# Performance work log

Hardware: AMD Instinct MI355X
Metric: run time of the kernel (lower is better)

The kernel has to match this reference:

```python
import jax, jax.numpy as jnp
import numpy as np

B, S, HID = 1, 2048, 2048
H, KV, D = 16, 4, 128  # head_dim = HID // H; GQA group size g = H // KV
THETA = 10000.0


def setup_inputs() -> dict:
    key = jax.random.key(0)
    ks = jax.random.split(key, 5)
    s = 0.02  # initializer_range
    return {
        "hidden_states": jax.random.normal(ks[0], (B, S, HID), jnp.float32),
        "wq": jax.random.normal(ks[1], (HID, H * D), jnp.float32) * s,
        "wk": jax.random.normal(ks[2], (HID, KV * D), jnp.float32) * s,
        "wv": jax.random.normal(ks[3], (HID, KV * D), jnp.float32) * s,
        "wo": jax.random.normal(ks[4], (H * D, HID), jnp.float32) * s,
        "attention_mask": jnp.ones((B, S), jnp.int32),
        "position_ids": jnp.broadcast_to(jnp.arange(S, dtype=jnp.int32), (B, S)),
    }


def _rope(x, position_ids):
    # x: [b, s, h, d]; rotate consecutive (even, odd) pairs by angle t * theta^{-2j/d}
    half = D // 2
    inv_freq = 1.0 / (THETA ** (jnp.arange(0, D, 2, dtype=jnp.float32) / D))  # [half]
    ang = position_ids[..., None].astype(jnp.float32) * inv_freq  # [b, s, half]
    cos = jnp.cos(ang)[:, :, None, :]  # [b, s, 1, half]
    sin = jnp.sin(ang)[:, :, None, :]
    xr = x.astype(jnp.float32).reshape(*x.shape[:-1], half, 2)
    x0, x1 = xr[..., 0], xr[..., 1]
    out = jnp.stack((x0 * cos - x1 * sin, x0 * sin + x1 * cos), axis=-1)
    return out.reshape(x.shape)


def reference(hidden_states, wq, wk, wv, wo, attention_mask, position_ids):
    b, s, _ = hidden_states.shape
    g = H // KV
    xq = (hidden_states @ wq).reshape(b, s, H, D)
    xk = (hidden_states @ wk).reshape(b, s, KV, D)
    xv = (hidden_states @ wv).reshape(b, s, KV, D)
    # GQA: each kv head repeated g consecutive times -> H heads (matches einops '(h g)')
    xk = jnp.repeat(xk, g, axis=2)
    xv = jnp.repeat(xv, g, axis=2)
    xq = _rope(xq, position_ids)
    xk = _rope(xk, position_ids)
    # causal + padding mask -> additive bias (0 or -inf), softmax in fp32
    causal = jnp.tril(jnp.ones((s, s), dtype=bool))[None, None]  # [1,1,q,k]
    mask = causal & (attention_mask[:, None, None, :] > 0)  # [b,1,q,k]
    scores = jnp.einsum('bqhd,bkhd->bhqk', xq.astype(jnp.float32), xk.astype(jnp.float32))
    scores = scores / jnp.sqrt(jnp.float32(D))
    scores = jnp.where(mask, scores, jnp.finfo(jnp.float32).min)
    attn_weights = jax.nn.softmax(scores, axis=-1)  # [b,h,q,k] fp32
    attn = jnp.einsum('bhqk,bkhd->bqhd', attn_weights, xv.astype(jnp.float32))
    return (attn.reshape(b, s, H * D).astype(hidden_states.dtype)) @ wo
```

## Files before the change

kernel.cpp:

```cpp
#include <hip/hip_runtime.h>
#include <hip/hip_bf16.h>

#define S_LEN 2048
#define HIDDIM 2048
#define NH 16
#define NKV 4
#define HD 128
#define KVROW 1024
#define QKVN 3072

typedef __attribute__((ext_vector_type(8))) short short8;
typedef __attribute__((ext_vector_type(8))) unsigned short ushort8;
typedef __attribute__((ext_vector_type(4))) float f32x4;

__device__ __forceinline__ unsigned short f2bf(float f) {
  union { float f; unsigned int u; } v; v.f = f;
  unsigned int r = (v.u + 0x7FFFu + ((v.u >> 16) & 1u)) >> 16;
  return (unsigned short)r;
}
__device__ __forceinline__ float bf2f(unsigned short h) {
  union { unsigned int u; float f; } v; v.u = ((unsigned int)h) << 16;
  return v.f;
}

__device__ __forceinline__ void gl2lds16(const unsigned short* src,
                                         unsigned short* dst) {
  __builtin_amdgcn_global_load_lds(
      (const __attribute__((address_space(1))) unsigned int*)src,
      (__attribute__((address_space(3))) unsigned int*)dst, 16, 0, 0);
}

__device__ __forceinline__ void tw_body(
    const float* __restrict__ W, unsigned short* __restrict__ Wt,
    int Nsrc, int Kdst, int n_off, int bx, int by, int tid,
    unsigned short (*Ts)[72]) {
  const int n0 = bx * 64, k0 = by * 64;
  const int c2 = (tid & 31) * 2, rb = tid >> 5;
#pragma unroll
  for (int p = 0; p < 8; ++p) {
    int r = rb + p * 8;
    float2 v = *(const float2*)&W[(size_t)(k0 + r) * Nsrc + n0 + c2];
    Ts[c2][r] = f2bf(v.x);
    Ts[c2 + 1][r] = f2bf(v.y);
  }
  __syncthreads();
  const int n = tid >> 2, kq = (tid & 3) * 16;
  ushort8 w0 = *(const ushort8*)&Ts[n][kq];
  ushort8 w1 = *(const ushort8*)&Ts[n][kq + 8];
  size_t base = (size_t)(n_off + n0 + n) * Kdst + k0 + kq;
  *(ushort8*)&Wt[base] = w0;
  *(ushort8*)&Wt[base + 8] = w1;
}

__global__ __launch_bounds__(256) void prep_kernel(
    const float* __restrict__ H, unsigned short* __restrict__ Hb,
    const float* __restrict__ wq, const float* __restrict__ wk,
    const float* __restrict__ wv, unsigned short* __restrict__ WT1,
    const int* __restrict__ amask, unsigned* __restrict__ mb) {
  __shared__ unsigned short Ts[64][72];
  const int b = (int)blockIdx.x, tid = threadIdx.x;
  if (b < 2048) {
    int i = (b * 256 + tid) * 8;
    float4 a = *(const float4*)(H + i), c = *(const float4*)(H + i + 4);
    ushort8 r;
    r[0] = f2bf(a.x); r[1] = f2bf(a.y); r[2] = f2bf(a.z); r[3] = f2bf(a.w);
    r[4] = f2bf(c.x); r[5] = f2bf(c.y); r[6] = f2bf(c.z); r[7] = f2bf(c.w);
    *(ushort8*)(Hb + i) = r;
  } else if (b < 3072) {
    int t = b - 2048;
    tw_body(wq, WT1, HIDDIM, HIDDIM, 0, t & 31, t >> 5, tid, Ts);
  } else if (b < 3328) {
    int t = b - 3072;
    tw_body(wk, WT1, 512, HIDDIM, 2048, t & 7, t >> 3, tid, Ts);
  } else if (b < 3584) {
    int t = b - 3328;
    tw_body(wv, WT1, 512, HIDDIM, 2560, t & 7, t >> 3, tid, Ts);
  } else {
    if (tid < 64) {
      unsigned m = 0;
#pragma unroll
      for (int i = 0; i < 32; ++i) m |= (amask[tid * 32 + i] != 0 ? 1u : 0u) << i;
      mb[tid] = m;
    }
  }
}

__global__ __launch_bounds__(256) void transpose_w(
    const float* __restrict__ W, unsigned short* __restrict__ Wt,
    int Nsrc, int Kdst, int n_off) {
  __shared__ unsigned short Ts[64][72];
  tw_body(W, Wt, Nsrc, Kdst, n_off, (int)blockIdx.x, (int)blockIdx.y,
          (int)threadIdx.x, Ts);
}

__global__ __launch_bounds__(256) void tvrope_kernel(
    unsigned short* __restrict__ Qb, unsigned short* __restrict__ KVb,
    unsigned short* __restrict__ Vt, const int* __restrict__ pos) {
  __shared__ unsigned short Ts[64][72];
  const int b = (int)blockIdx.x, tid = threadIdx.x;
  if (b < 256) {
    const int c0 = (b & 7) * 64, s0 = (b >> 3) * 64;
    const int sr = tid >> 2, cq = (tid & 3) * 16;
    ushort8 a = *(const ushort8*)&KVb[(size_t)(s0 + sr) * KVROW + 512 + c0 + cq];
    ushort8 c = *(const ushort8*)&KVb[(size_t)(s0 + sr) * KVROW + 512 + c0 + cq + 8];
#pragma unroll
    for (int j = 0; j < 8; ++j) { Ts[cq + j][sr] = a[j]; Ts[cq + 8 + j][sr] = c[j]; }
    __syncthreads();
    const int cc = tid >> 2, sq = (tid & 3) * 16;
    ushort8 w0 = *(const ushort8*)&Ts[cc][sq];
    ushort8 w1 = *(const ushort8*)&Ts[cc][sq + 8];
    *(ushort8*)&Vt[(size_t)(c0 + cc) * S_LEN + s0 + sq] = w0;
    *(ushort8*)&Vt[(size_t)(c0 + cc) * S_LEN + s0 + sq + 8] = w1;
  } else {
    int idx = (b - 256) * 256 + tid;
    int s = idx >> 6, j = idx & 63;
    float inv = exp2f(-0.2076205059304703f * (float)j);
    float ang = (float)pos[s] * inv;
    float sn, cs;
    __sincosf(ang, &sn, &cs);
    auto rot = [&](unsigned short* base) {
      unsigned* p = (unsigned*)base;
      unsigned v = *p;
      float x0 = bf2f((unsigned short)(v & 0xffff));
      float x1 = bf2f((unsigned short)(v >> 16));
      unsigned r = (unsigned)f2bf(x0 * cs - x1 * sn) |
                   ((unsigned)f2bf(x0 * sn + x1 * cs) << 16);
      *p = r;
    };
#pragma unroll
    for (int hh = 0; hh < NH; ++hh) rot(Qb + (size_t)s * HIDDIM + hh * HD + 2 * j);
#pragma unroll
    for (int hh = 0; hh < NKV; ++hh) rot(KVb + (size_t)s * KVROW + hh * HD + 2 * j);
  }
}

template <bool CF>
__global__ __launch_bounds__(256) void gemm_tn(
    const unsigned short* __restrict__ A, const unsigned short* __restrict__ Bt,
    void* __restrict__ C1, void* __restrict__ C2,
    int M, int N, int K, int splitcol, int ld1, int ld2) {
  __shared__ unsigned short As[2][128 * 64];
  __shared__ unsigned short Bs[2][64 * 64];
  const int m0 = blockIdx.y * 128, n0 = blockIdx.x * 64;
  const int tid = threadIdx.x, wid = tid >> 6, lane = tid & 63;
  const int wr = wid >> 1, wc = wid & 1;
  const int lr = lane & 15, lg = lane >> 4;

  f32x4 acc[4][2];
#pragma unroll
  for (int m = 0; m < 4; ++m)
#pragma unroll
    for (int n = 0; n < 2; ++n) acc[m][n] = (f32x4){0.f, 0.f, 0.f, 0.f};

  const int srow = lane >> 3;
  const int scolb = (lane & 7) << 4;
  auto stage = [&](int k0, int b) {
#pragma unroll
    for (int j = 0; j < 4; ++j) {
      int row = wid * 32 + j * 8 + srow;
      int src = (scolb ^ ((row & 7) << 4)) >> 1;
      gl2lds16(A + (size_t)(m0 + row) * K + k0 + src,
               &As[b][(wid * 32 + j * 8) * 64]);
    }
#pragma unroll
    for (int j = 0; j < 2; ++j) {
      int row = wid * 16 + j * 8 + srow;
      int src = (scolb ^ ((row & 7) << 4)) >> 1;
      gl2lds16(Bt + (size_t)(n0 + row) * K + k0 + src,
               &Bs[b][(wid * 16 + j * 8) * 64]);
    }
  };

  stage(0, 0);
  int cur = 0;
  for (int k0 = 0; k0 < K; k0 += 64) {
    __syncthreads();
    if (k0 + 64 < K) stage(k0 + 64, cur ^ 1);
#pragma unroll
    for (int s = 0; s < 2; ++s) {
      short8 af[4], bfv[2];
#pragma unroll
      for (int m = 0; m < 4; ++m) {
        int row = wr * 64 + m * 16 + lr;
        int off = ((s * 64 + lg * 16) ^ ((row & 7) << 4)) >> 1;
        af[m] = *(const short8*)&As[cur][row * 64 + off];
      }
#pragma unroll
      for (int n = 0; n < 2; ++n) {
        int row = wc * 32 + n * 16 + lr;
        int off = ((s * 64 + lg * 16) ^ ((row & 7) << 4)) >> 1;
        bfv[n] = *(const short8*)&Bs[cur][row * 64 + off];
      }
#pragma unroll
      for (int m = 0; m < 4; ++m)
#pragma unroll
        for (int n = 0; n < 2; ++n)
          acc[m][n] = __builtin_amdgcn_mfma_f32_16x16x32_bf16(af[m], bfv[n], acc[m][n], 0, 0, 0);
    }
    cur ^= 1;
  }

#pragma unroll
  for (int m = 0; m < 4; ++m)
#pragma unroll
    for (int n = 0; n < 2; ++n)
#pragma unroll
      for (int r = 0; r < 4; ++r) {
        int row = m0 + wr * 64 + m * 16 + lg * 4 + r;
        int col = n0 + wc * 32 + n * 16 + lr;
        float v = acc[m][n][r];
        if (CF) ((float*)C1)[(size_t)row * ld1 + col] = v;
        else if (col < splitcol) ((unsigned short*)C1)[(size_t)row * ld1 + col] = f2bf(v);
        else ((unsigned short*)C2)[(size_t)row * ld2 + (col - splitcol)] = f2bf(v);
      }
}

__global__ __launch_bounds__(256) void attn_kernel(
    const unsigned short* __restrict__ Qb, const unsigned short* __restrict__ KVb,
    const unsigned short* __restrict__ VtG, const unsigned* __restrict__ mbits,
    unsigned short* __restrict__ Ob,
    unsigned short* __restrict__ Opart, float* __restrict__ Lpart, int nsplit) {
  const int x = (int)blockIdx.x;
  const int qt = 63 - (x >> 2);
  const int c = x & 3;
  const int kvh = (int)blockIdx.y;
  const int nch = (qt >> 4) + 1;
  if (nsplit == 0) { if (c != 0) return; }
  else if (c >= nch) return;
  const int qb = qt * 32;
  int kbeg = 0, kend = qb + 32;
  bool partial = false;
  if (nsplit && nch > 1) {
    kbeg = c * 512;
    kend = min(kend, kbeg + 512);
    partial = true;
  }

  __shared__ unsigned short Klds[2][32 * 128];
  __shared__ unsigned short Vlds[2][128 * 32];
  const int tid = threadIdx.x, wid = tid >> 6, lane = tid & 63;
  const int lr = lane & 15, lg = lane >> 4;
  const int h = kvh * 4 + wid;

  short8 qfa[4], qfb[4];
  {
    const unsigned short* qpa = Qb + (size_t)(qb + lr) * HIDDIM + h * HD;
    const unsigned short* qpb = Qb + (size_t)(qb + 16 + lr) * HIDDIM + h * HD;
#pragma unroll
    for (int cc = 0; cc < 4; ++cc) {
      qfa[cc] = *(const short8*)(qpa + cc * 32 + lg * 8);
      qfb[cc] = *(const short8*)(qpb + cc * 32 + lg * 8);
    }
  }
  f32x4 oa[8], ob[8];
#pragma unroll
  for (int cc = 0; cc < 8; ++cc) {
    oa[cc] = (f32x4){0.f, 0.f, 0.f, 0.f};
    ob[cc] = (f32x4){0.f, 0.f, 0.f, 0.f};
  }
  float lsa = 0.f, lsb = 0.f;

  const unsigned short* Vg = VtG + (size_t)(kvh * HD) * S_LEN;

  const int ksr_ = lane >> 4;
  const int kscb = (lane & 15) << 4;
  const int vsr_ = lane >> 2;
  const int vscb = (lane & 3) << 4;

  auto stage = [&](int kt, int b) {
#pragma unroll
    for (int j = 0; j < 2; ++j) {
      int krow = wid * 8 + j * 4 + ksr_;
      int ksrc = (kscb ^ ((krow & 7) << 4)) >> 1;
      gl2lds16(KVb + (size_t)(kt + krow) * KVROW + kvh * HD + ksrc,
               &Klds[b][(wid * 8 + j * 4) * 128]);
      int vrow = wid * 32 + j * 16 + vsr_;
      int vsrc = (vscb ^ ((vrow & 3) << 4)) >> 1;
      gl2lds16(Vg + (size_t)vrow * S_LEN + kt + vsrc,
               &Vlds[b][(wid * 32 + j * 16) * 32]);
    }
  };

  stage(kbeg, 0);

  const int qra = qb + lr, qrb = qb + 16 + lr;
  const float SCALE = 0.08838834764831845f;
  int cur = 0;

  const int s0 = lr + ((lg & 1) << 5);
  const int s1 = s0 + 16;
  const bool lo = (lg < 2);
  auto exchange = [&](const float p[2][4]) -> short8 {
    unsigned W0 = (unsigned)f2bf(p[0][0]) | ((unsigned)f2bf(p[0][1]) << 16);
    unsigned W1 = (unsigned)f2bf(p[0][2]) | ((unsigned)f2bf(p[0][3]) << 16);
    unsigned W2 = (unsigned)f2bf(p[1][0]) | ((unsigned)f2bf(p[1][1]) << 16);
    unsigned W3 = (unsigned)f2bf(p[1][2]) | ((unsigned)f2bf(p[1][3]) << 16);
    unsigned x0 = __shfl(W0, s0, 64), y0 = __shfl(W2, s0, 64);
    unsigned x1 = __shfl(W1, s0, 64), y1 = __shfl(W3, s0, 64);
    unsigned x2 = __shfl(W0, s1, 64), y2 = __shfl(W2, s1, 64);
    unsigned x3 = __shfl(W1, s1, 64), y3 = __shfl(W3, s1, 64);
    union { unsigned u[4]; short8 s8; } pu;
    pu.u[0] = lo ? x0 : y0;
    pu.u[1] = lo ? x1 : y1;
    pu.u[2] = lo ? x2 : y2;
    pu.u[3] = lo ? x3 : y3;
    return pu.s8;
  };

  for (int kt = kbeg; kt < kend; kt += 32) {
    __syncthreads();
    if (kt + 32 < kend) stage(kt + 32, cur ^ 1);

    f32x4 sa[2], sb[2];
#pragma unroll
    for (int t = 0; t < 2; ++t) {
      sa[t] = (f32x4){0.f, 0.f, 0.f, 0.f};
      sb[t] = (f32x4){0.f, 0.f, 0.f, 0.f};
    }
    const unsigned short* kbase = &Klds[cur][0];
    __builtin_amdgcn_s_setprio(1);
#pragma unroll
    for (int t = 0; t < 2; ++t)
#pragma unroll
      for (int cc = 0; cc < 4; ++cc) {
        short8 kf = *(const short8*)(kbase + ((t * 16 + lr) << 7) +
                                     ((((cc << 6) + (lg << 4)) ^ ((lr & 7) << 4)) >> 1));
        sa[t] = __builtin_amdgcn_mfma_f32_16x16x32_bf16(kf, qfa[cc], sa[t], 0, 0, 0);
        sb[t] = __builtin_amdgcn_mfma_f32_16x16x32_bf16(kf, qfb[cc], sb[t], 0, 0, 0);
      }
    __builtin_amdgcn_s_setprio(0);
    const unsigned mw = mbits[kt >> 5];
    float pa[2][4], pb[2][4];
    if ((kt + 31 <= qb) && (mw == ~0u)) {
#pragma unroll
      for (int t = 0; t < 2; ++t)
#pragma unroll
        for (int r = 0; r < 4; ++r) {
          float va = __expf(sa[t][r] * SCALE - 3.0f);
          float vb = __expf(sb[t][r] * SCALE - 3.0f);
          pa[t][r] = va; lsa += va;
          pb[t][r] = vb; lsb += vb;
        }
    } else {
#pragma unroll
      for (int t = 0; t < 2; ++t)
#pragma unroll
        for (int r = 0; r < 4; ++r) {
          int kk = t * 16 + lg * 4 + r;
          bool okm = (mw >> kk) & 1u;
          float va = __expf((okm && kt + kk <= qra) ? sa[t][r] * SCALE - 3.0f : -1e30f);
          float vb = __expf((okm && kt + kk <= qrb) ? sb[t][r] * SCALE - 3.0f : -1e30f);
          pa[t][r] = va; lsa += va;
          pb[t][r] = vb; lsb += vb;
        }
    }
    short8 pfa = exchange(pa);
    short8 pfb = exchange(pb);
    const unsigned short* vbase = &Vlds[cur][0];
    __builtin_amdgcn_s_setprio(1);
#pragma unroll
    for (int cc = 0; cc < 8; ++cc) {
      short8 vf = *(const short8*)(vbase + ((cc * 16 + lr) << 5) +
                                   ((lg ^ (lr & 3)) << 3));
      oa[cc] = __builtin_amdgcn_mfma_f32_16x16x32_bf16(pfa, vf, oa[cc], 0, 0, 0);
      ob[cc] = __builtin_amdgcn_mfma_f32_16x16x32_bf16(pfb, vf, ob[cc], 0, 0, 0);
    }
    __builtin_amdgcn_s_setprio(0);
    cur ^= 1;
  }

  float la = lsa;
  la += __shfl_xor(la, 16, 64);
  la += __shfl_xor(la, 32, 64);
  float lb = lsb;
  lb += __shfl_xor(lb, 16, 64);
  lb += __shfl_xor(lb, 32, 64);

  if (!partial) {
    float lra[4], lrb[4];
#pragma unroll
    for (int r = 0; r < 4; ++r) {
      lra[r] = 1.0f / __shfl(la, lg * 4 + r, 16);
      lrb[r] = 1.0f / __shfl(lb, lg * 4 + r, 16);
    }
#pragma unroll
    for (int cc = 0; cc < 8; ++cc)
#pragma unroll
      for (int r = 0; r < 4; ++r) {
        const int rowa = qb + lg * 4 + r;
        const int rowb = qb + 16 + lg * 4 + r;
        Ob[(size_t)rowa * HIDDIM + h * HD + cc * 16 + lr] = f2bf(oa[cc][r] * lra[r]);
        Ob[(size_t)rowb * HIDDIM + h * HD + cc * 16 + lr] = f2bf(ob[cc][r] * lrb[r]);
      }
  } else {
    const int g = qt >> 4, j = qt & 15;
    const int base = (g == 1) ? 0 : (g == 2) ? 32 : 80;
    const int slot = base + j * nch + c + 144 * kvh;
    if (lg == 0) {
      Lpart[slot * 128 + wid * 32 + lr] = la;
      Lpart[slot * 128 + wid * 32 + 16 + lr] = lb;
    }
#pragma unroll
    for (int cc = 0; cc < 8; ++cc)
#pragma unroll
      for (int r = 0; r < 4; ++r) {
        Opart[(size_t)slot * 16384 + wid * 4096 +
              (lg * 4 + r) * 128 + cc * 16 + lr] = f2bf(oa[cc][r]);
        Opart[(size_t)slot * 16384 + wid * 4096 +
              (16 + lg * 4 + r) * 128 + cc * 16 + lr] = f2bf(ob[cc][r]);
      }
  }
}

__global__ __launch_bounds__(256) void combine_kernel(
    const unsigned short* __restrict__ Opart, const float* __restrict__ Lpart,
    unsigned short* __restrict__ Ab) {
  const int qt = 16 + (int)blockIdx.x;
  const int kvh = (int)blockIdx.y;
  const int nch = (qt >> 4) + 1;
  const int g = qt >> 4, j = qt & 15;
  const int base = (g == 1) ? 0 : (g == 2) ? 32 : 80;
  const int s0 = base + j * nch + 144 * kvh;
  const int tid = threadIdx.x;
  const int rowid = tid >> 1;
  const int d0 = (tid & 1) * 64;
  float L = 0.f;
  for (int cc = 0; cc < nch; ++cc) L += Lpart[(s0 + cc) * 128 + rowid];
  const float linv = 1.0f / L;
  const int h = kvh * 4 + (rowid >> 5);
  const int row = qt * 32 + (rowid & 31);
  unsigned short* dst = Ab + (size_t)row * HIDDIM + h * HD + d0;
  for (int i = 0; i < 64; i += 8) {
    float acc[8] = {0, 0, 0, 0, 0, 0, 0, 0};
    for (int cc = 0; cc < nch; ++cc) {
      ushort8 v = *(const ushort8*)&Opart[(size_t)(s0 + cc) * 16384 +
                                          rowid * 128 + d0 + i];
#pragma unroll
      for (int k = 0; k < 8; ++k) acc[k] += bf2f(v[k]);
    }
    ushort8 r;
#pragma unroll
    for (int k = 0; k < 8; ++k) r[k] = f2bf(acc[k] * linv);
    *(ushort8*)(dst + i) = r;
  }
}

extern "C" void kernel_launch(void* const* d_in, const int* in_sizes, int n_in,
                              void* d_out, int out_size, void* d_ws, size_t ws_size,
                              hipStream_t stream) {
  const float* hidden = (const float*)d_in[0];
  const float* wq = (const float*)d_in[1];
  const float* wk = (const float*)d_in[2];
  const float* wv = (const float*)d_in[3];
  const float* wo = (const float*)d_in[4];
  const int* amask = (const int*)d_in[5];
  const int* pos = (const int*)d_in[6];

  unsigned short* Qb = (unsigned short*)d_ws;
  unsigned short* KVb = Qb + (size_t)S_LEN * HIDDIM;
  unsigned short* Ab = KVb + (size_t)S_LEN * KVROW;
  unsigned short* WT1 = Ab + (size_t)S_LEN * HIDDIM;
  unsigned short* Hb = WT1 + (size_t)QKVN * HIDDIM;
  float* out = (float*)d_out;

  unsigned short* Opart = WT1;
  unsigned short* Vt_chunk = WT1 + (size_t)576 * 16384;
  unsigned* mbits_chunk = (unsigned*)((char*)d_ws + 41943040ull);
  float* Lpart = (float*)((char*)d_ws + 41943296ull);
  const size_t need_chunk = 42238208ull;
  unsigned short* Vt_fb = WT1 + (size_t)HIDDIM * HIDDIM;
  unsigned* mbits_fb = (unsigned*)((char*)d_ws + 31457280ull);

  const int nsplit = (ws_size >= need_chunk) ? 1 : 0;
  unsigned short* Vt = nsplit ? Vt_chunk : Vt_fb;
  unsigned* mbits = nsplit ? mbits_chunk : mbits_fb;

  dim3 blk(256);
  prep_kernel<<<3585, blk, 0, stream>>>(hidden, Hb, wq, wk, wv, WT1, amask, mbits);
  gemm_tn<false><<<dim3(QKVN / 64, S_LEN / 128), blk, 0, stream>>>(
      Hb, WT1, Qb, KVb, S_LEN, QKVN, HIDDIM, 2048, HIDDIM, KVROW);
  tvrope_kernel<<<768, blk, 0, stream>>>(Qb, KVb, Vt, pos);
  attn_kernel<<<dim3(256, NKV), blk, 0, stream>>>(
      Qb, KVb, Vt, mbits, Ab, Opart, Lpart, nsplit);
  if (nsplit)
    combine_kernel<<<dim3(48, NKV), blk, 0, stream>>>(Opart, Lpart, Ab);
  transpose_w<<<dim3(32, 32), blk, 0, stream>>>(wo, WT1, HIDDIM, HIDDIM, 0);
  gemm_tn<true><<<dim3(HIDDIM / 64, S_LEN / 128), blk, 0, stream>>>(
      Ab, WT1, out, nullptr, S_LEN, HIDDIM, HIDDIM, HIDDIM, HIDDIM, 0);
}
```

Baseline: 162.3 us.

## Widen attention KV tile to 64 and pass P through LDS instead of shuffles

Each pipeline stage of the attention kernel now loads a 64-key K/V tile into double-buffered LDS and runs two 32-key sub-steps per barrier, which halves the number of __syncthreads and staging rounds. The bf16 probability fragment exchange, previously done with cross-lane shuffles, now writes to a per-wave padded LDS scratch and reads back in MFMA operand layout. This raises LDS use, which may lower occupancy, and adds LDS traffic for P. The P store and load within a wave rely on no explicit wave barrier.

```diff
diff --git a/kernel.cpp b/kernel.cpp
--- a/kernel.cpp
+++ b/kernel.cpp
@@ -11,6 +11,7 @@
 
 typedef __attribute__((ext_vector_type(8))) short short8;
 typedef __attribute__((ext_vector_type(8))) unsigned short ushort8;
+typedef __attribute__((ext_vector_type(4))) unsigned short ushort4v;
 typedef __attribute__((ext_vector_type(4))) float f32x4;
 
 __device__ __forceinline__ unsigned short f2bf(float f) {
@@ -236,8 +237,9 @@
     partial = true;
   }
 
-  __shared__ unsigned short Klds[2][32 * 128];
-  __shared__ unsigned short Vlds[2][128 * 32];
+  __shared__ unsigned short Klds[2][64 * 128];
+  __shared__ unsigned short Vlds[2][128 * 64];
+  __shared__ unsigned short Plds[4][32][40];
   const int tid = threadIdx.x, wid = tid >> 6, lane = tid & 63;
   const int lr = lane & 15, lg = lane >> 4;
   const int h = kvh * 4 + wid;
@@ -262,22 +264,17 @@
 
   const unsigned short* Vg = VtG + (size_t)(kvh * HD) * S_LEN;
 
-  const int ksr_ = lane >> 4;
-  const int kscb = (lane & 15) << 4;
-  const int vsr_ = lane >> 2;
-  const int vscb = (lane & 3) << 4;
-
   auto stage = [&](int kt, int b) {
 #pragma unroll
-    for (int j = 0; j < 2; ++j) {
-      int krow = wid * 8 + j * 4 + ksr_;
-      int ksrc = (kscb ^ ((krow & 7) << 4)) >> 1;
+    for (int j = 0; j < 4; ++j) {
+      int krow = wid * 16 + j * 4 + (lane >> 4);
+      int ksrc = ((((lane & 15) << 4) ^ ((krow & 7) << 4))) >> 1;
       gl2lds16(KVb + (size_t)(kt + krow) * KVROW + kvh * HD + ksrc,
-               &Klds[b][(wid * 8 + j * 4) * 128]);
-      int vrow = wid * 32 + j * 16 + vsr_;
-      int vsrc = (vscb ^ ((vrow & 3) << 4)) >> 1;
+               &Klds[b][(wid * 16 + j * 4) * 128]);
+      int vrow = wid * 32 + j * 8 + (lane >> 3);
+      int vsrc = ((((lane & 7) << 4) ^ ((vrow & 7) << 4))) >> 1;
       gl2lds16(Vg + (size_t)vrow * S_LEN + kt + vsrc,
-               &Vlds[b][(wid * 32 + j * 16) * 32]);
+               &Vlds[b][(wid * 32 + j * 8) * 64]);
     }
   };
 
@@ -287,85 +284,81 @@
   const float SCALE = 0.08838834764831845f;
   int cur = 0;
 
-  const int s0 = lr + ((lg & 1) << 5);
-  const int s1 = s0 + 16;
-  const bool lo = (lg < 2);
-  auto exchange = [&](const float p[2][4]) -> short8 {
-    unsigned W0 = (unsigned)f2bf(p[0][0]) | ((unsigned)f2bf(p[0][1]) << 16);
-    unsigned W1 = (unsigned)f2bf(p[0][2]) | ((unsigned)f2bf(p[0][3]) << 16);
-    unsigned W2 = (unsigned)f2bf(p[1][0]) | ((unsigned)f2bf(p[1][1]) << 16);
-    unsigned W3 = (unsigned)f2bf(p[1][2]) | ((unsigned)f2bf(p[1][3]) << 16);
-    unsigned x0 = __shfl(W0, s0, 64), y0 = __shfl(W2, s0, 64);
-    unsigned x1 = __shfl(W1, s0, 64), y1 = __shfl(W3, s0, 64);
-    unsigned x2 = __shfl(W0, s1, 64), y2 = __shfl(W2, s1, 64);
-    unsigned x3 = __shfl(W1, s1, 64), y3 = __shfl(W3, s1, 64);
-    union { unsigned u[4]; short8 s8; } pu;
-    pu.u[0] = lo ? x0 : y0;
-    pu.u[1] = lo ? x1 : y1;
-    pu.u[2] = lo ? x2 : y2;
-    pu.u[3] = lo ? x3 : y3;
-    return pu.s8;
-  };
-
-  for (int kt = kbeg; kt < kend; kt += 32) {
+  for (int kt = kbeg; kt < kend; kt += 64) {
     __syncthreads();
-    if (kt + 32 < kend) stage(kt + 32, cur ^ 1);
-
-    f32x4 sa[2], sb[2];
-#pragma unroll
-    for (int t = 0; t < 2; ++t) {
-      sa[t] = (f32x4){0.f, 0.f, 0.f, 0.f};
-      sb[t] = (f32x4){0.f, 0.f, 0.f, 0.f};
-    }
-    const unsigned short* kbase = &Klds[cur][0];
-    __builtin_amdgcn_s_setprio(1);
-#pragma unroll
-    for (int t = 0; t < 2; ++t)
-#pragma unroll
-      for (int cc = 0; cc < 4; ++cc) {
-        short8 kf = *(const short8*)(kbase + ((t * 16 + lr) << 7) +
-                                     ((((cc << 6) + (lg << 4)) ^ ((lr & 7) << 4)) >> 1));
-        sa[t] = __builtin_amdgcn_mfma_f32_16x16x32_bf16(kf, qfa[cc], sa[t], 0, 0, 0);
-        sb[t] = __builtin_amdgcn_mfma_f32_16x16x32_bf16(kf, qfb[cc], sb[t], 0, 0, 0);
-      }
-    __builtin_amdgcn_s_setprio(0);
-    const unsigned mw = mbits[kt >> 5];
-    float pa[2][4], pb[2][4];
-    if ((kt + 31 <= qb) && (mw == ~0u)) {
+    if (kt + 64 < kend) stage(kt + 64, cur ^ 1);
+
+#pragma unroll
+    for (int s = 0; s < 2; ++s) {
+      const int kts = kt + s * 32;
+      if (kts >= kend) break;
+
+      f32x4 sa[2], sb[2];
+#pragma unroll
+      for (int t = 0; t < 2; ++t) {
+        sa[t] = (f32x4){0.f, 0.f, 0.f, 0.f};
+        sb[t] = (f32x4){0.f, 0.f, 0.f, 0.f};
+      }
+      const unsigned short* kbase = &Klds[cur][0];
+      __builtin_amdgcn_s_setprio(1);
 #pragma unroll
       for (int t = 0; t < 2; ++t)
 #pragma unroll
-        for (int r = 0; r < 4; ++r) {
-          float va = __expf(sa[t][r] * SCALE - 3.0f);
-          float vb = __expf(sb[t][r] * SCALE - 3.0f);
-          pa[t][r] = va; lsa += va;
-          pb[t][r] = vb; lsb += vb;
+        for (int cc = 0; cc < 4; ++cc) {
+          int krow = s * 32 + t * 16 + lr;
+          short8 kf = *(const short8*)(kbase + (krow << 7) +
+                                       ((((cc << 6) + (lg << 4)) ^ ((krow & 7) << 4)) >> 1));
+          sa[t] = __builtin_amdgcn_mfma_f32_16x16x32_bf16(kf, qfa[cc], sa[t], 0, 0, 0);
+          sb[t] = __builtin_amdgcn_mfma_f32_16x16x32_bf16(kf, qfb[cc], sb[t], 0, 0, 0);
         }
-    } else {
-#pragma unroll
-      for (int t = 0; t < 2; ++t)
-#pragma unroll
-        for (int r = 0; r < 4; ++r) {
-          int kk = t * 16 + lg * 4 + r;
-          bool okm = (mw >> kk) & 1u;
-          float va = __expf((okm && kt + kk <= qra) ? sa[t][r] * SCALE - 3.0f : -1e30f);
-          float vb = __expf((okm && kt + kk <= qrb) ? sb[t][r] * SCALE - 3.0f : -1e30f);
-          pa[t][r] = va; lsa += va;
-          pb[t][r] = vb; lsb += vb;
-        }
-    }
-    short8 pfa = exchange(pa);
-    short8 pfb = exchange(pb);
-    const unsigned short* vbase = &Vlds[cur][0];
-    __builtin_amdgcn_s_setprio(1);
-#pragma unroll
-    for (int cc = 0; cc < 8; ++cc) {
-      short8 vf = *(const short8*)(vbase + ((cc * 16 + lr) << 5) +
-                                   ((lg ^ (lr & 3)) << 3));
-      oa[cc] = __builtin_amdgcn_mfma_f32_16x16x32_bf16(pfa, vf, oa[cc], 0, 0, 0);
-      ob[cc] = __builtin_amdgcn_mfma_f32_16x16x32_bf16(pfb, vf, ob[cc], 0, 0, 0);
-    }
-    __builtin_amdgcn_s_setprio(0);
+      __builtin_amdgcn_s_setprio(0);
+      const unsigned mw = mbits[kts >> 5];
+      float pa[2][4], pb[2][4];
+      if ((kts + 31 <= qb) && (mw == ~0u)) {
+#pragma unroll
+        for (int t = 0; t < 2; ++t)
+#pragma unroll
+          for (int r = 0; r < 4; ++r) {
+            float va = __expf(sa[t][r] * SCALE - 3.0f);
+            float vb = __expf(sb[t][r] * SCALE - 3.0f);
+            pa[t][r] = va; lsa += va;
+            pb[t][r] = vb; lsb += vb;
+          }
+      } else {
+#pragma unroll
+        for (int t = 0; t < 2; ++t)
+#pragma unroll
+          for (int r = 0; r < 4; ++r) {
+            int kk = t * 16 + lg * 4 + r;
+            bool okm = (mw >> kk) & 1u;
+            float va = __expf((okm && kts + kk <= qra) ? sa[t][r] * SCALE - 3.0f : -1e30f);
+            float vb = __expf((okm && kts + kk <= qrb) ? sb[t][r] * SCALE - 3.0f : -1e30f);
+            pa[t][r] = va; lsa += va;
+            pb[t][r] = vb; lsb += vb;
+          }
+      }
+#pragma unroll
+      for (int t = 0; t < 2; ++t) {
+        ushort4v pka, pkb;
+#pragma unroll
+        for (int r = 0; r < 4; ++r) { pka[r] = f2bf(pa[t][r]); pkb[r] = f2bf(pb[t][r]); }
+        *(ushort4v*)&Plds[wid][lr][t * 16 + lg * 4] = pka;
+        *(ushort4v*)&Plds[wid][16 + lr][t * 16 + lg * 4] = pkb;
+      }
+      short8 pfa = *(const short8*)&Plds[wid][lr][lg * 8];
+      short8 pfb = *(const short8*)&Plds[wid][16 + lr][lg * 8];
+      const unsigned short* vbase = &Vlds[cur][0];
+      __builtin_amdgcn_s_setprio(1);
+#pragma unroll
+      for (int cc = 0; cc < 8; ++cc) {
+        int vrow = cc * 16 + lr;
+        short8 vf = *(const short8*)(vbase + (vrow << 6) +
+                                     (((s * 64 + (lg << 4)) ^ ((vrow & 7) << 4)) >> 1));
+        oa[cc] = __builtin_amdgcn_mfma_f32_16x16x32_bf16(pfa, vf, oa[cc], 0, 0, 0);
+        ob[cc] = __builtin_amdgcn_mfma_f32_16x16x32_bf16(pfb, vf, ob[cc], 0, 0, 0);
+      }
+      __builtin_amdgcn_s_setprio(0);
+    }
     cur ^= 1;
   }
 
```

New measurement: 182.8 us. +12.6%, slower.

## Fold wo transpose into prep kernel and route P through LDS

Applied to the files above, without the earlier changes.

When the workspace is large enough, the wo weight transpose/bf16 conversion moves into the prep kernel, writing to a separate buffer so the standalone transpose launch is skipped. The attention-mask bit packing moves from prep into the rope kernel. In attention, the shuffle-based exchange of P fragments into MFMA operand layout is replaced by a store to and reload from a per-wave LDS tile. This saves one launch and replaces the cross-lane shuffles with LDS traffic, at the cost of extra shared memory and a larger prep grid.

```diff
diff --git a/kernel.cpp b/kernel.cpp
--- a/kernel.cpp
+++ b/kernel.cpp
@@ -11,6 +11,7 @@
 
 typedef __attribute__((ext_vector_type(8))) short short8;
 typedef __attribute__((ext_vector_type(8))) unsigned short ushort8;
+typedef __attribute__((ext_vector_type(4))) unsigned short ushort4v;
 typedef __attribute__((ext_vector_type(4))) float f32x4;
 
 __device__ __forceinline__ unsigned short f2bf(float f) {
@@ -56,7 +57,7 @@
     const float* __restrict__ H, unsigned short* __restrict__ Hb,
     const float* __restrict__ wq, const float* __restrict__ wk,
     const float* __restrict__ wv, unsigned short* __restrict__ WT1,
-    const int* __restrict__ amask, unsigned* __restrict__ mb) {
+    const float* __restrict__ wo, unsigned short* __restrict__ WoT) {
   __shared__ unsigned short Ts[64][72];
   const int b = (int)blockIdx.x, tid = threadIdx.x;
   if (b < 2048) {
@@ -76,12 +77,8 @@
     int t = b - 3328;
     tw_body(wv, WT1, 512, HIDDIM, 2560, t & 7, t >> 3, tid, Ts);
   } else {
-    if (tid < 64) {
-      unsigned m = 0;
-#pragma unroll
-      for (int i = 0; i < 32; ++i) m |= (amask[tid * 32 + i] != 0 ? 1u : 0u) << i;
-      mb[tid] = m;
-    }
+    int t = b - 3584;
+    tw_body(wo, WoT, HIDDIM, HIDDIM, 0, t & 31, t >> 5, tid, Ts);
   }
 }
 
@@ -95,7 +92,8 @@
 
 __global__ __launch_bounds__(256) void tvrope_kernel(
     unsigned short* __restrict__ Qb, unsigned short* __restrict__ KVb,
-    unsigned short* __restrict__ Vt, const int* __restrict__ pos) {
+    unsigned short* __restrict__ Vt, const int* __restrict__ pos,
+    const int* __restrict__ amask, unsigned* __restrict__ mb) {
   __shared__ unsigned short Ts[64][72];
   const int b = (int)blockIdx.x, tid = threadIdx.x;
   if (b < 256) {
@@ -111,7 +109,7 @@
     ushort8 w1 = *(const ushort8*)&Ts[cc][sq + 8];
     *(ushort8*)&Vt[(size_t)(c0 + cc) * S_LEN + s0 + sq] = w0;
     *(ushort8*)&Vt[(size_t)(c0 + cc) * S_LEN + s0 + sq + 8] = w1;
-  } else {
+  } else if (b < 768) {
     int idx = (b - 256) * 256 + tid;
     int s = idx >> 6, j = idx & 63;
     float inv = exp2f(-0.2076205059304703f * (float)j);
@@ -131,6 +129,13 @@
     for (int hh = 0; hh < NH; ++hh) rot(Qb + (size_t)s * HIDDIM + hh * HD + 2 * j);
 #pragma unroll
     for (int hh = 0; hh < NKV; ++hh) rot(KVb + (size_t)s * KVROW + hh * HD + 2 * j);
+  } else {
+    if (tid < 64) {
+      unsigned m = 0;
+#pragma unroll
+      for (int i = 0; i < 32; ++i) m |= (amask[tid * 32 + i] != 0 ? 1u : 0u) << i;
+      mb[tid] = m;
+    }
   }
 }
 
@@ -238,6 +243,7 @@
 
   __shared__ unsigned short Klds[2][32 * 128];
   __shared__ unsigned short Vlds[2][128 * 32];
+  __shared__ unsigned short Plds[4][32][40];
   const int tid = threadIdx.x, wid = tid >> 6, lane = tid & 63;
   const int lr = lane & 15, lg = lane >> 4;
   const int h = kvh * 4 + wid;
@@ -287,26 +293,6 @@
   const float SCALE = 0.08838834764831845f;
   int cur = 0;
 
-  const int s0 = lr + ((lg & 1) << 5);
-  const int s1 = s0 + 16;
-  const bool lo = (lg < 2);
-  auto exchange = [&](const float p[2][4]) -> short8 {
-    unsigned W0 = (unsigned)f2bf(p[0][0]) | ((unsigned)f2bf(p[0][1]) << 16);
-    unsigned W1 = (unsigned)f2bf(p[0][2]) | ((unsigned)f2bf(p[0][3]) << 16);
-    unsigned W2 = (unsigned)f2bf(p[1][0]) | ((unsigned)f2bf(p[1][1]) << 16);
-    unsigned W3 = (unsigned)f2bf(p[1][2]) | ((unsigned)f2bf(p[1][3]) << 16);
-    unsigned x0 = __shfl(W0, s0, 64), y0 = __shfl(W2, s0, 64);
-    unsigned x1 = __shfl(W1, s0, 64), y1 = __shfl(W3, s0, 64);
-    unsigned x2 = __shfl(W0, s1, 64), y2 = __shfl(W2, s1, 64);
-    unsigned x3 = __shfl(W1, s1, 64), y3 = __shfl(W3, s1, 64);
-    union { unsigned u[4]; short8 s8; } pu;
-    pu.u[0] = lo ? x0 : y0;
-    pu.u[1] = lo ? x1 : y1;
-    pu.u[2] = lo ? x2 : y2;
-    pu.u[3] = lo ? x3 : y3;
-    return pu.s8;
-  };
-
   for (int kt = kbeg; kt < kend; kt += 32) {
     __syncthreads();
     if (kt + 32 < kend) stage(kt + 32, cur ^ 1);
@@ -354,8 +340,16 @@
           pb[t][r] = vb; lsb += vb;
         }
     }
-    short8 pfa = exchange(pa);
-    short8 pfb = exchange(pb);
+#pragma unroll
+    for (int t = 0; t < 2; ++t) {
+      ushort4v pka, pkb;
+#pragma unroll
+      for (int r = 0; r < 4; ++r) { pka[r] = f2bf(pa[t][r]); pkb[r] = f2bf(pb[t][r]); }
+      *(ushort4v*)&Plds[wid][lr][t * 16 + lg * 4] = pka;
+      *(ushort4v*)&Plds[wid][16 + lr][t * 16 + lg * 4] = pkb;
+    }
+    short8 pfa = *(const short8*)&Plds[wid][lr][lg * 8];
+    short8 pfb = *(const short8*)&Plds[wid][16 + lr][lg * 8];
     const unsigned short* vbase = &Vlds[cur][0];
     __builtin_amdgcn_s_setprio(1);
 #pragma unroll
@@ -468,23 +462,29 @@
   unsigned* mbits_chunk = (unsigned*)((char*)d_ws + 41943040ull);
   float* Lpart = (float*)((char*)d_ws + 41943296ull);
   const size_t need_chunk = 42238208ull;
+  unsigned short* WoT2 = (unsigned short*)((char*)d_ws + 42238208ull);
+  const size_t need_tier2 = 42238208ull + 8388608ull;
   unsigned short* Vt_fb = WT1 + (size_t)HIDDIM * HIDDIM;
   unsigned* mbits_fb = (unsigned*)((char*)d_ws + 31457280ull);
 
   const int nsplit = (ws_size >= need_chunk) ? 1 : 0;
+  const int tier2 = (ws_size >= need_tier2) ? 1 : 0;
   unsigned short* Vt = nsplit ? Vt_chunk : Vt_fb;
   unsigned* mbits = nsplit ? mbits_chunk : mbits_fb;
+  unsigned short* WoT = tier2 ? WoT2 : WT1;
 
   dim3 blk(256);
-  prep_kernel<<<3585, blk, 0, stream>>>(hidden, Hb, wq, wk, wv, WT1, amask, mbits);
+  prep_kernel<<<tier2 ? 4608 : 3584, blk, 0, stream>>>(
+      hidden, Hb, wq, wk, wv, WT1, wo, WoT2);
   gemm_tn<false><<<dim3(QKVN / 64, S_LEN / 128), blk, 0, stream>>>(
       Hb, WT1, Qb, KVb, S_LEN, QKVN, HIDDIM, 2048, HIDDIM, KVROW);
-  tvrope_kernel<<<768, blk, 0, stream>>>(Qb, KVb, Vt, pos);
+  tvrope_kernel<<<769, blk, 0, stream>>>(Qb, KVb, Vt, pos, amask, mbits);
   attn_kernel<<<dim3(256, NKV), blk, 0, stream>>>(
       Qb, KVb, Vt, mbits, Ab, Opart, Lpart, nsplit);
   if (nsplit)
     combine_kernel<<<dim3(48, NKV), blk, 0, stream>>>(Opart, Lpart, Ab);
-  transpose_w<<<dim3(32, 32), blk, 0, stream>>>(wo, WT1, HIDDIM, HIDDIM, 0);
+  if (!tier2)
+    transpose_w<<<dim3(32, 32), blk, 0, stream>>>(wo, WT1, HIDDIM, HIDDIM, 0);
   gemm_tn<true><<<dim3(HIDDIM / 64, S_LEN / 128), blk, 0, stream>>>(
-      Ab, WT1, out, nullptr, S_LEN, HIDDIM, HIDDIM, HIDDIM, HIDDIM, 0);
-}
+      Ab, WoT, out, nullptr, S_LEN, HIDDIM, HIDDIM, HIDDIM, HIDDIM, 0);
+}
```

Result: faster. 155.1 us (-4.5%).
